# Kernel tuning notes

Hardware: AMD Instinct MI355X
Metric: run time of the kernel (lower is better)

Reference implementation:

```python
import jax, jax.numpy as jnp
import numpy as np
from jax import lax


def setup_inputs() -> dict:
    key = jax.random.key(0)
    ks = jax.random.split(key, 8)
    b, l, d_model = 2, 1024, 768
    expand, d_state, d_conv = 2, 16, 4
    d_inner = d_model * expand            # 1536
    dt_rank = -(-d_model // 16)           # ceil(768/16) = 48
    x = jax.random.normal(ks[0], (b, l, d_model), jnp.float32)
    W_in = jax.random.normal(ks[1], (d_model, 2 * d_inner), jnp.float32) * 0.02
    conv_w = jax.random.normal(ks[2], (d_inner, 1, d_conv), jnp.float32) * 0.1
    conv_b = jnp.zeros((d_inner,), jnp.float32)
    W_x = jax.random.normal(ks[3], (d_inner, dt_rank + 2 * d_state), jnp.float32) * 0.02
    W_dt = jax.random.normal(ks[4], (dt_rank, d_inner), jnp.float32) * 0.02
    b_dt = jax.random.normal(ks[5], (d_inner,), jnp.float32) * 0.02
    # A_log = log(1..d_state) broadcast over d_inner, as in the module init
    A_log = jnp.broadcast_to(jnp.log(jnp.arange(1, d_state + 1, dtype=jnp.float32)), (d_inner, d_state)).copy()
    D = jnp.ones((d_inner,), jnp.float32)
    W_out = jax.random.normal(ks[6], (d_inner, d_model), jnp.float32) * 0.02
    return {"x": x, "W_in": W_in, "conv_w": conv_w, "conv_b": conv_b, "W_x": W_x,
            "W_dt": W_dt, "b_dt": b_dt, "A_log": A_log, "D": D, "W_out": W_out}


def _silu(v):
    return v * jax.nn.sigmoid(v)


def reference(x, W_in, conv_w, conv_b, W_x, W_dt, b_dt, A_log, D, W_out):
    b, l, d_model = x.shape
    d_inner, _, d_conv = conv_w.shape
    dt_rank = W_dt.shape[0]
    n = A_log.shape[1]

    # in_proj and split into x / res paths
    x_and_res = x @ W_in                              # (b, l, 2*d_inner)
    xi, res = jnp.split(x_and_res, 2, axis=-1)

    # depthwise causal conv1d (torch pads d_conv-1 both sides then slices [:l])
    xc = jnp.transpose(xi, (0, 2, 1))                 # (b, d_inner, l)
    xc = lax.conv_general_dilated(
        xc, conv_w, window_strides=(1,), padding=[(d_conv - 1, 0)],
        dimension_numbers=("NCH", "OIH", "NCH"), feature_group_count=d_inner)
    xc = xc + conv_b[None, :, None]
    u = _silu(jnp.transpose(xc, (0, 2, 1)))           # (b, l, d_inner)

    # SSM parameters (input-dependent)
    A = -jnp.exp(A_log.astype(jnp.float32))           # (d_inner, n)
    x_dbl = u @ W_x                                   # (b, l, dt_rank + 2n)
    delta = x_dbl[..., :dt_rank]
    B = x_dbl[..., dt_rank:dt_rank + n]               # (b, l, n)
    C = x_dbl[..., dt_rank + n:]                      # (b, l, n)
    delta = jax.nn.softplus(delta @ W_dt + b_dt)      # (b, l, d_inner)

    # discretize
    deltaA = jnp.exp(delta[..., None] * A)            # (b, l, d_inner, n)
    deltaB_u = delta[..., None] * B[:, :, None, :] * u[..., None]  # (b, l, d_inner, n)

    # parallel associative scan over l: h_t = deltaA_t * h_{t-1} + deltaB_u_t
    def combine(c1, c2):
        a1, b1 = c1
        a2, b2 = c2
        return (a1 * a2, a2 * b1 + b2)

    _, hs = lax.associative_scan(combine, (deltaA, deltaB_u), axis=1)  # (b, l, d_inner, n)

    y = jnp.einsum("bldn,bln->bld", hs, C) + u * D    # (b, l, d_inner)
    y = y * _silu(res)
    out = y @ W_out                                   # (b, l, d_model)
    return out
```

## Files before the change

### kernel.cpp

```cpp
#include <hip/hip_runtime.h>
#include <math.h>

#define DI 1536
#define DM 768
#define NSTATE 16
#define DTRANK 48
#define LSEQ 1024
#define NBATCH 2
#define MROWS (NBATCH*LSEQ)
#define NXR 3072
#define NCHUNK 128
#define CLEN 8
#define SCB 128
#define DMP 16

typedef __attribute__((ext_vector_type(4))) float f32x4;
typedef __attribute__((ext_vector_type(8))) short s16x8;
typedef __attribute__((ext_vector_type(4))) unsigned int u32x4;

__device__ __forceinline__ unsigned short f2bf(float f) {
  unsigned int x = __builtin_bit_cast(unsigned int, f);
  return (unsigned short)((x + 0x7fffu + ((x >> 16) & 1u)) >> 16);
}
__device__ __forceinline__ float bf2f(unsigned short b) {
  unsigned int u = ((unsigned int)b) << 16;
  return __builtin_bit_cast(float, u);
}

__device__ __forceinline__ void gload_lds16(const void* g, void* l) {
  __builtin_amdgcn_global_load_lds(
      (const __attribute__((address_space(1))) void*)g,
      (__attribute__((address_space(3))) void*)l, 16, 0, 0);
}

__global__ __launch_bounds__(256) void prep_kernel(
    const float* __restrict__ x, const float* __restrict__ W_in,
    const float* __restrict__ W_out, const float* __restrict__ W_x,
    const float* __restrict__ A_log,
    unsigned short* __restrict__ x_bf, unsigned short* __restrict__ WinT,
    unsigned short* __restrict__ WoutT, unsigned short* __restrict__ WxT,
    float* __restrict__ negA)
{
  __shared__ float t[32][33];
  const int bid = blockIdx.x;
  const int tid = threadIdx.x;
  if (bid < 768) {
    long i = ((long)bid * 256 + tid) * 8;
    f32x4 v0 = *(const f32x4*)&x[i];
    f32x4 v1 = *(const f32x4*)&x[i + 4];
    unsigned short o[8];
    #pragma unroll
    for (int j = 0; j < 4; ++j) { o[j] = f2bf(v0[j]); o[4 + j] = f2bf(v1[j]); }
    *(u32x4*)&x_bf[i] = *(u32x4*)o;
    return;
  }
  int tx = tid & 31, ty = tid >> 5;
  if (bid >= 4368) {
    int rtile = (bid - 4368) * 32;
    #pragma unroll
    for (int i = 0; i < 4; ++i) {
      int r = ty + i * 8;
      if (tx < 16) t[r][tx] = A_log[(long)(rtile + r) * NSTATE + tx];
    }
    __syncthreads();
    #pragma unroll
    for (int i = 0; i < 2; ++i) {
      int cc = ty + i * 8;
      negA[(long)cc * DI + rtile + tx] = -__expf(t[tx][cc]);
    }
    return;
  }
  const float* in; unsigned short* out; int R, C, bx, by; bool guard = false;
  if (bid < 3072)      { int q = bid - 768;  in = W_in;  out = WinT;  R = DM; C = NXR; bx = q % 96; by = q / 96; }
  else if (bid < 4224) { int q = bid - 3072; in = W_out; out = WoutT; R = DI; C = DM;  bx = q % 24; by = q / 24; }
  else                 { int q = bid - 4224; in = W_x;   out = WxT;   R = DI; C = 80;  bx = q % 3;  by = q / 3; guard = true; }
  int ctile = bx * 32, rtile = by * 32;
  #pragma unroll
  for (int i = 0; i < 4; ++i) {
    int r = ty + i * 8;
    if (!guard || (rtile + r < R && ctile + tx < C))
      t[r][tx] = in[(long)(rtile + r) * C + ctile + tx];
  }
  __syncthreads();
  #pragma unroll
  for (int i = 0; i < 4; ++i) {
    int cc = ty + i * 8;
    if (!guard || (ctile + cc < C && rtile + tx < R))
      out[(long)(ctile + cc) * R + rtile + tx] = f2bf(t[tx][cc]);
  }
}

template<int FM, int FN, bool SPLIT>
__global__ __launch_bounds__(256) void gemm_bf16(
    const unsigned short* __restrict__ A,
    const unsigned short* __restrict__ BT,
    float* __restrict__ C,
    unsigned short* __restrict__ res_bf,
    int M, int N, int K)
{
  constexpr int BM = 32 * FM, BN = 32 * FN;
  constexpr int TM = BM / 16, TN = BN / 16;
  __shared__ unsigned short Ap[BM * 32];
  __shared__ unsigned short Bp[BN * 32];
  const int tid = threadIdx.x;
  const int lane = tid & 63, wave = tid >> 6;
  const int wr = wave >> 1, wc = wave & 1;
  const int lg = lane >> 4, lr = lane & 15;
  const int m0 = blockIdx.y * BM, n0 = blockIdx.x * BN;
  f32x4 acc[FM][FN] = {};
  for (int k0 = 0; k0 < K; k0 += 32) {
    #pragma unroll
    for (int p = 0; p < TM / 4; ++p) {
      int tile = wave + p * 4;
      gload_lds16(&A[(long)(m0 + tile * 16 + lr) * K + k0 + lg * 8], &Ap[tile * 512]);
    }
    #pragma unroll
    for (int p = 0; p < TN / 4; ++p) {
      int tile = wave + p * 4;
      gload_lds16(&BT[(long)(n0 + tile * 16 + lr) * K + k0 + lg * 8], &Bp[tile * 512]);
    }
    __syncthreads();
    s16x8 af[FM], bfr[FN];
    #pragma unroll
    for (int m = 0; m < FM; ++m)
      af[m] = *(s16x8*)&Ap[(((wr * FM + m) * 4 + lg) * 16 + lr) * 8];
    #pragma unroll
    for (int n = 0; n < FN; ++n)
      bfr[n] = *(s16x8*)&Bp[(((wc * FN + n) * 4 + lg) * 16 + lr) * 8];
    #pragma unroll
    for (int m = 0; m < FM; ++m)
      #pragma unroll
      for (int n = 0; n < FN; ++n)
        acc[m][n] = __builtin_amdgcn_mfma_f32_16x16x32_bf16(af[m], bfr[n], acc[m][n], 0, 0, 0);
    __syncthreads();
  }
  #pragma unroll
  for (int m = 0; m < FM; ++m)
    #pragma unroll
    for (int n = 0; n < FN; ++n)
      #pragma unroll
      for (int r = 0; r < 4; ++r) {
        int row = m0 + wr * 16 * FM + m * 16 + lg * 4 + r;
        int col = n0 + wc * 16 * FN + n * 16 + lr;
        if (SPLIT) {
          if (n0 < DI) C[(long)row * DI + col] = acc[m][n][r];
          else res_bf[(long)row * DI + col - DI] = f2bf(acc[m][n][r]);
        } else {
          C[(long)row * N + col] = acc[m][n][r];
        }
      }
}

__global__ __launch_bounds__(256) void conv_silu_kernel(
    const float* __restrict__ xi,
    const float* __restrict__ conv_w,
    const float* __restrict__ conv_b,
    unsigned short* __restrict__ u_bf)
{
  int idx = blockIdx.x * 256 + threadIdx.x;
  if (idx >= MROWS * DI) return;
  int c = idx % DI;
  int m = idx / DI;
  int t = m % LSEQ;
  float w0 = conv_w[c * 4 + 0], w1 = conv_w[c * 4 + 1];
  float w2 = conv_w[c * 4 + 2], w3 = conv_w[c * 4 + 3];
  float acc = conv_b[c];
  if (t >= 3) acc = fmaf(xi[(long)(m - 3) * DI + c], w0, acc);
  if (t >= 2) acc = fmaf(xi[(long)(m - 2) * DI + c], w1, acc);
  if (t >= 1) acc = fmaf(xi[(long)(m - 1) * DI + c], w2, acc);
  acc = fmaf(xi[(long)m * DI + c], w3, acc);
  float s = acc / (1.f + __expf(-acc));
  u_bf[idx] = f2bf(s);
}

__global__ __launch_bounds__(256) void xdbl_mfma(
    const unsigned short* __restrict__ u_bf,
    const unsigned short* __restrict__ WxT,
    float* __restrict__ xdbl)
{
  const int tid = threadIdx.x;
  const int lane = tid & 63, wave = tid >> 6;
  const int lg = lane >> 4, lr = lane & 15;
  const int m0 = blockIdx.x * 16;
  f32x4 acc[5] = {};
  const int kbase = wave * (DI / 4);
  #pragma unroll
  for (int kk = 0; kk < DI / 4; kk += 32) {
    int k0 = kbase + kk;
    s16x8 af = *(const s16x8*)&u_bf[(long)(m0 + lr) * DI + k0 + lg * 8];
    #pragma unroll
    for (int n = 0; n < 5; ++n) {
      s16x8 bfr = *(const s16x8*)&WxT[(long)(n * 16 + lr) * DI + k0 + lg * 8];
      acc[n] = __builtin_amdgcn_mfma_f32_16x16x32_bf16(af, bfr, acc[n], 0, 0, 0);
    }
  }
  __shared__ float red[4][16][80];
  #pragma unroll
  for (int n = 0; n < 5; ++n)
    #pragma unroll
    for (int r = 0; r < 4; ++r)
      red[wave][lg * 4 + r][n * 16 + lr] = acc[n][r];
  __syncthreads();
  for (int i = tid; i < 16 * 80; i += 256) {
    int row = i / 80, col = i % 80;
    float s = red[0][row][col] + red[1][row][col] + red[2][row][col] + red[3][row][col];
    xdbl[(long)(m0 + row) * 80 + col] = s;
  }
}

__global__ __launch_bounds__(256) void delta_kernel(
    const float* __restrict__ xdbl,
    const float* __restrict__ W_dt,
    const float* __restrict__ b_dt,
    float* __restrict__ delta)
{
  __shared__ float sx[DMP][DTRANK];
  const int tid = threadIdx.x;
  const int c = blockIdx.x * 256 + tid;
  const int m0 = blockIdx.y * DMP;
  for (int i = tid; i < DMP * DTRANK; i += 256) {
    int mm = i / DTRANK, r = i % DTRANK;
    sx[mm][r] = xdbl[(long)(m0 + mm) * 80 + r];
  }
  __syncthreads();
  float bias = b_dt[c];
  float acc[DMP];
  #pragma unroll
  for (int mm = 0; mm < DMP; ++mm) acc[mm] = bias;
  for (int r = 0; r < DTRANK; ++r) {
    float wv = W_dt[(long)r * DI + c];
    #pragma unroll
    for (int mm = 0; mm < DMP; ++mm)
      acc[mm] = fmaf(sx[mm][r], wv, acc[mm]);
  }
  #pragma unroll
  for (int mm = 0; mm < DMP; ++mm) {
    float v = acc[mm];
    float sp = (v > 20.f) ? v : log1pf(__expf(v));
    delta[(long)(m0 + mm) * DI + c] = sp;
  }
}

__global__ __launch_bounds__(SCB) void scan_ph1(
    const float* __restrict__ delta,
    const float* __restrict__ xdbl,
    const unsigned short* __restrict__ u_bf,
    const float* __restrict__ negA,
    float* __restrict__ Aprod,
    float* __restrict__ Hend)
{
  const int b = blockIdx.z, chunk = blockIdx.y;
  const int tid = threadIdx.x;
  const int d = blockIdx.x * SCB + tid;
  const long mbase = (long)b * LSEQ + chunk * CLEN;
  __shared__ float sB[CLEN][NSTATE];
  for (int i = tid; i < CLEN * NSTATE; i += SCB) {
    int t = i >> 4, j = i & 15;
    sB[t][j] = xdbl[(mbase + t) * 80 + DTRANK + j];
  }
  __syncthreads();
  float a[NSTATE];
  #pragma unroll
  for (int n = 0; n < NSTATE; ++n)
    a[n] = negA[(long)n * DI + d];
  float h[NSTATE] = {};
  float Ap[NSTATE];
  #pragma unroll
  for (int n = 0; n < NSTATE; ++n) Ap[n] = 1.f;
  #pragma unroll
  for (int t = 0; t < CLEN; ++t) {
    long m = mbase + t;
    float dt = delta[m * DI + d];
    float uu = bf2f(u_bf[m * DI + d]);
    float dtu = dt * uu;
    #pragma unroll
    for (int n = 0; n < NSTATE; ++n) {
      float dA = __expf(dt * a[n]);
      Ap[n] *= dA;
      h[n] = fmaf(dA, h[n], dtu * sB[t][n]);
    }
  }
  const long o = ((long)(b * NCHUNK + chunk) * NSTATE) * DI + d;
  #pragma unroll
  for (int n = 0; n < NSTATE; ++n) {
    Aprod[o + (long)n * DI] = Ap[n];
    Hend[o + (long)n * DI] = h[n];
  }
}

__global__ __launch_bounds__(256) void scan_ph2(
    const float* __restrict__ Aprod,
    float* __restrict__ Hend)
{
  int idx = blockIdx.x * 256 + threadIdx.x;
  int b = idx / (DI * NSTATE);
  int r = idx % (DI * NSTATE);
  long o = (long)b * NCHUNK * DI * NSTATE + r;
  const long stride = (long)DI * NSTATE;
  float h = 0.f;
  for (int c = 0; c < NCHUNK; ++c) {
    float Ap = Aprod[o + c * stride];
    float He = Hend[o + c * stride];
    Hend[o + c * stride] = h;
    h = fmaf(Ap, h, He);
  }
}

__global__ __launch_bounds__(SCB) void scan_ph3(
    const float* __restrict__ delta,
    const float* __restrict__ xdbl,
    const unsigned short* __restrict__ u_bf,
    const unsigned short* __restrict__ res_bf,
    const float* __restrict__ negA,
    const float* __restrict__ Dp,
    const float* __restrict__ Hstart,
    unsigned short* __restrict__ yg)
{
  const int b = blockIdx.z, chunk = blockIdx.y;
  const int tid = threadIdx.x;
  const int d = blockIdx.x * SCB + tid;
  const long mbase = (long)b * LSEQ + chunk * CLEN;
  __shared__ float sB[CLEN][NSTATE], sC[CLEN][NSTATE];
  for (int i = tid; i < CLEN * NSTATE; i += SCB) {
    int t = i >> 4, j = i & 15;
    long mo = (mbase + t) * 80 + DTRANK + j;
    sB[t][j] = xdbl[mo];
    sC[t][j] = xdbl[mo + NSTATE];
  }
  __syncthreads();
  float a[NSTATE];
  #pragma unroll
  for (int n = 0; n < NSTATE; ++n)
    a[n] = negA[(long)n * DI + d];
  const float Dv = Dp[d];
  const long o = ((long)(b * NCHUNK + chunk) * NSTATE) * DI + d;
  float h[NSTATE];
  #pragma unroll
  for (int n = 0; n < NSTATE; ++n)
    h[n] = Hstart[o + (long)n * DI];
  #pragma unroll
  for (int t = 0; t < CLEN; ++t) {
    long m = mbase + t;
    float dt = delta[m * DI + d];
    float uu = bf2f(u_bf[m * DI + d]);
    float rr = bf2f(res_bf[m * DI + d]);
    float dtu = dt * uu;
    float p0 = 0.f, p1 = 0.f, p2 = 0.f, p3 = 0.f;
    #pragma unroll
    for (int q = 0; q < 4; ++q) {
      float dA0 = __expf(dt * a[q*4+0]);
      float dA1 = __expf(dt * a[q*4+1]);
      float dA2 = __expf(dt * a[q*4+2]);
      float dA3 = __expf(dt * a[q*4+3]);
      h[q*4+0] = fmaf(dA0, h[q*4+0], dtu * sB[t][q*4+0]);
      h[q*4+1] = fmaf(dA1, h[q*4+1], dtu * sB[t][q*4+1]);
      h[q*4+2] = fmaf(dA2, h[q*4+2], dtu * sB[t][q*4+2]);
      h[q*4+3] = fmaf(dA3, h[q*4+3], dtu * sB[t][q*4+3]);
    }
    #pragma unroll
    for (int n = 0; n < NSTATE; n += 4) {
      p0 = fmaf(h[n+0], sC[t][n+0], p0);
      p1 = fmaf(h[n+1], sC[t][n+1], p1);
      p2 = fmaf(h[n+2], sC[t][n+2], p2);
      p3 = fmaf(h[n+3], sC[t][n+3], p3);
    }
    float yv = (p0 + p1) + (p2 + p3) + uu * Dv;
    float gate = rr / (1.f + __expf(-rr));
    yg[m * DI + d] = f2bf(yv * gate);
  }
}

extern "C" void kernel_launch(void* const* d_in, const int* in_sizes, int n_in,
                              void* d_out, int out_size, void* d_ws, size_t ws_size,
                              hipStream_t stream)
{
  const float* x      = (const float*)d_in[0];
  const float* W_in   = (const float*)d_in[1];
  const float* conv_w = (const float*)d_in[2];
  const float* conv_b = (const float*)d_in[3];
  const float* W_x    = (const float*)d_in[4];
  const float* W_dt   = (const float*)d_in[5];
  const float* b_dt   = (const float*)d_in[6];
  const float* A_log  = (const float*)d_in[7];
  const float* Dp     = (const float*)d_in[8];
  const float* W_out  = (const float*)d_in[9];
  float* out = (float*)d_out;

  char* p = (char*)d_ws;
  float* xi     = (float*)(p + 0);
  unsigned short* res_bf = (unsigned short*)(p + 12582912);
  unsigned short* u_bf   = (unsigned short*)(p + 18874368);
  float* xdbl   = (float*)(p + 25165824);
  float* delta  = (float*)(p + 25821184);
  float* Aprod  = (float*)(p + 38404096);
  float* Hend   = (float*)(p + 63569920);
  unsigned short* yg    = (unsigned short*)(p + 88735744);
  unsigned short* x_bf  = (unsigned short*)(p + 95027200);
  unsigned short* WinT  = (unsigned short*)(p + 98172928);
  unsigned short* WoutT = (unsigned short*)(p + 102891520);
  unsigned short* WxT   = (unsigned short*)(p + 105250816);
  float* negA   = (float*)(p + 105496576);

  prep_kernel<<<4416, 256, 0, stream>>>(x, W_in, W_out, W_x, A_log,
                                        x_bf, WinT, WoutT, WxT, negA);
  gemm_bf16<2, 4, true><<<dim3(NXR / 128, MROWS / 64), 256, 0, stream>>>(
      x_bf, WinT, xi, res_bf, MROWS, NXR, DM);
  conv_silu_kernel<<<(MROWS * DI + 255) / 256, 256, 0, stream>>>(
      xi, conv_w, conv_b, u_bf);
  xdbl_mfma<<<MROWS / 16, 256, 0, stream>>>(u_bf, WxT, xdbl);
  delta_kernel<<<dim3(DI / 256, MROWS / DMP), 256, 0, stream>>>(xdbl, W_dt, b_dt, delta);
  scan_ph1<<<dim3(DI / SCB, NCHUNK, NBATCH), SCB, 0, stream>>>(
      delta, xdbl, u_bf, negA, Aprod, Hend);
  scan_ph2<<<(NBATCH * DI * NSTATE) / 256, 256, 0, stream>>>(Aprod, Hend);
  scan_ph3<<<dim3(DI / SCB, NCHUNK, NBATCH), SCB, 0, stream>>>(
      delta, xdbl, u_bf, res_bf, negA, Dp, Hend, yg);
  gemm_bf16<2, 2, false><<<dim3(DM / 64, MROWS / 64), 256, 0, stream>>>(
      yg, WoutT, out, nullptr, MROWS, DM, DI);
}
```

Before: 160.7 us.

## Fuse conv+SiLU into x_dbl MFMA kernel and vectorize LDS reads

Merges the depthwise conv+SiLU kernel with the x_dbl projection. Each block computes its 16 rows of u into padded LDS and still writes u_bf to global, then feeds the MFMA from LDS instead of re-reading global memory. This removes one launch and a global round-trip for u. The delta and scan kernels now read shared B/C/x_dbl values as aligned float4 vectors. The fused kernel runs only 128 blocks for the elementwise conv work, so parallelism for that phase drops.

```diff
diff --git a/kernel.cpp b/kernel.cpp
--- a/kernel.cpp
+++ b/kernel.cpp
@@ -13,6 +13,7 @@
 #define CLEN 8
 #define SCB 128
 #define DMP 16
+#define ULDS 1544
 
 typedef __attribute__((ext_vector_type(4))) float f32x4;
 typedef __attribute__((ext_vector_type(8))) short s16x8;
@@ -151,59 +152,61 @@
       }
 }
 
-__global__ __launch_bounds__(256) void conv_silu_kernel(
+__global__ __launch_bounds__(256) void mid_kernel(
     const float* __restrict__ xi,
     const float* __restrict__ conv_w,
     const float* __restrict__ conv_b,
-    unsigned short* __restrict__ u_bf)
-{
-  int idx = blockIdx.x * 256 + threadIdx.x;
-  if (idx >= MROWS * DI) return;
-  int c = idx % DI;
-  int m = idx / DI;
-  int t = m % LSEQ;
-  float w0 = conv_w[c * 4 + 0], w1 = conv_w[c * 4 + 1];
-  float w2 = conv_w[c * 4 + 2], w3 = conv_w[c * 4 + 3];
-  float acc = conv_b[c];
-  if (t >= 3) acc = fmaf(xi[(long)(m - 3) * DI + c], w0, acc);
-  if (t >= 2) acc = fmaf(xi[(long)(m - 2) * DI + c], w1, acc);
-  if (t >= 1) acc = fmaf(xi[(long)(m - 1) * DI + c], w2, acc);
-  acc = fmaf(xi[(long)m * DI + c], w3, acc);
-  float s = acc / (1.f + __expf(-acc));
-  u_bf[idx] = f2bf(s);
-}
-
-__global__ __launch_bounds__(256) void xdbl_mfma(
-    const unsigned short* __restrict__ u_bf,
     const unsigned short* __restrict__ WxT,
+    unsigned short* __restrict__ u_bf,
     float* __restrict__ xdbl)
 {
-  const int tid = threadIdx.x;
+  __shared__ __align__(16) char smem[16 * ULDS * 2];
+  unsigned short* uL = (unsigned short*)smem;
+  float* red = (float*)smem;
+  const int tid = threadIdx.x;
+  const int m0 = blockIdx.x * 16;
+  for (int i = tid; i < 16 * DI; i += 256) {
+    int row = i / DI, col = i - row * DI;
+    int m = m0 + row;
+    int t = m % LSEQ;
+    float w0 = conv_w[col * 4 + 0], w1 = conv_w[col * 4 + 1];
+    float w2 = conv_w[col * 4 + 2], w3 = conv_w[col * 4 + 3];
+    float acc = conv_b[col];
+    if (t >= 3) acc = fmaf(xi[(long)(m - 3) * DI + col], w0, acc);
+    if (t >= 2) acc = fmaf(xi[(long)(m - 2) * DI + col], w1, acc);
+    if (t >= 1) acc = fmaf(xi[(long)(m - 1) * DI + col], w2, acc);
+    acc = fmaf(xi[(long)m * DI + col], w3, acc);
+    float s = acc / (1.f + __expf(-acc));
+    unsigned short bv = f2bf(s);
+    uL[row * ULDS + col] = bv;
+    u_bf[(long)m * DI + col] = bv;
+  }
+  __syncthreads();
   const int lane = tid & 63, wave = tid >> 6;
   const int lg = lane >> 4, lr = lane & 15;
-  const int m0 = blockIdx.x * 16;
   f32x4 acc[5] = {};
   const int kbase = wave * (DI / 4);
   #pragma unroll
   for (int kk = 0; kk < DI / 4; kk += 32) {
     int k0 = kbase + kk;
-    s16x8 af = *(const s16x8*)&u_bf[(long)(m0 + lr) * DI + k0 + lg * 8];
+    s16x8 af = *(const s16x8*)&uL[lr * ULDS + k0 + lg * 8];
     #pragma unroll
     for (int n = 0; n < 5; ++n) {
       s16x8 bfr = *(const s16x8*)&WxT[(long)(n * 16 + lr) * DI + k0 + lg * 8];
       acc[n] = __builtin_amdgcn_mfma_f32_16x16x32_bf16(af, bfr, acc[n], 0, 0, 0);
     }
   }
-  __shared__ float red[4][16][80];
+  __syncthreads();
   #pragma unroll
   for (int n = 0; n < 5; ++n)
     #pragma unroll
     for (int r = 0; r < 4; ++r)
-      red[wave][lg * 4 + r][n * 16 + lr] = acc[n][r];
+      red[(wave * 16 + lg * 4 + r) * 80 + n * 16 + lr] = acc[n][r];
   __syncthreads();
   for (int i = tid; i < 16 * 80; i += 256) {
-    int row = i / 80, col = i % 80;
-    float s = red[0][row][col] + red[1][row][col] + red[2][row][col] + red[3][row][col];
+    int row = i / 80, col = i - row * 80;
+    float s = red[(0 * 16 + row) * 80 + col] + red[(1 * 16 + row) * 80 + col]
+            + red[(2 * 16 + row) * 80 + col] + red[(3 * 16 + row) * 80 + col];
     xdbl[(long)(m0 + row) * 80 + col] = s;
   }
 }
@@ -214,7 +217,7 @@
     const float* __restrict__ b_dt,
     float* __restrict__ delta)
 {
-  __shared__ float sx[DMP][DTRANK];
+  __shared__ __align__(16) float sx[DMP][DTRANK];
   const int tid = threadIdx.x;
   const int c = blockIdx.x * 256 + tid;
   const int m0 = blockIdx.y * DMP;
@@ -227,11 +230,19 @@
   float acc[DMP];
   #pragma unroll
   for (int mm = 0; mm < DMP; ++mm) acc[mm] = bias;
-  for (int r = 0; r < DTRANK; ++r) {
-    float wv = W_dt[(long)r * DI + c];
-    #pragma unroll
-    for (int mm = 0; mm < DMP; ++mm)
-      acc[mm] = fmaf(sx[mm][r], wv, acc[mm]);
+  for (int r = 0; r < DTRANK; r += 4) {
+    float wv0 = W_dt[(long)(r + 0) * DI + c];
+    float wv1 = W_dt[(long)(r + 1) * DI + c];
+    float wv2 = W_dt[(long)(r + 2) * DI + c];
+    float wv3 = W_dt[(long)(r + 3) * DI + c];
+    #pragma unroll
+    for (int mm = 0; mm < DMP; ++mm) {
+      f32x4 s4 = *(const f32x4*)&sx[mm][r];
+      float a = fmaf(s4[0], wv0, acc[mm]);
+      a = fmaf(s4[1], wv1, a);
+      a = fmaf(s4[2], wv2, a);
+      acc[mm] = fmaf(s4[3], wv3, a);
+    }
   }
   #pragma unroll
   for (int mm = 0; mm < DMP; ++mm) {
@@ -253,7 +264,7 @@
   const int tid = threadIdx.x;
   const int d = blockIdx.x * SCB + tid;
   const long mbase = (long)b * LSEQ + chunk * CLEN;
-  __shared__ float sB[CLEN][NSTATE];
+  __shared__ __align__(16) float sB[CLEN][NSTATE];
   for (int i = tid; i < CLEN * NSTATE; i += SCB) {
     int t = i >> 4, j = i & 15;
     sB[t][j] = xdbl[(mbase + t) * 80 + DTRANK + j];
@@ -274,10 +285,15 @@
     float uu = bf2f(u_bf[m * DI + d]);
     float dtu = dt * uu;
     #pragma unroll
-    for (int n = 0; n < NSTATE; ++n) {
-      float dA = __expf(dt * a[n]);
-      Ap[n] *= dA;
-      h[n] = fmaf(dA, h[n], dtu * sB[t][n]);
+    for (int q = 0; q < 4; ++q) {
+      f32x4 b4 = *(const f32x4*)&sB[t][q * 4];
+      #pragma unroll
+      for (int j = 0; j < 4; ++j) {
+        int n = q * 4 + j;
+        float dA = __expf(dt * a[n]);
+        Ap[n] *= dA;
+        h[n] = fmaf(dA, h[n], dtu * b4[j]);
+      }
     }
   }
   const long o = ((long)(b * NCHUNK + chunk) * NSTATE) * DI + d;
@@ -320,7 +336,7 @@
   const int tid = threadIdx.x;
   const int d = blockIdx.x * SCB + tid;
   const long mbase = (long)b * LSEQ + chunk * CLEN;
-  __shared__ float sB[CLEN][NSTATE], sC[CLEN][NSTATE];
+  __shared__ __align__(16) float sB[CLEN][NSTATE], sC[CLEN][NSTATE];
   for (int i = tid; i < CLEN * NSTATE; i += SCB) {
     int t = i >> 4, j = i & 15;
     long mo = (mbase + t) * 80 + DTRANK + j;
@@ -348,21 +364,23 @@
     float p0 = 0.f, p1 = 0.f, p2 = 0.f, p3 = 0.f;
     #pragma unroll
     for (int q = 0; q < 4; ++q) {
+      f32x4 b4 = *(const f32x4*)&sB[t][q * 4];
       float dA0 = __expf(dt * a[q*4+0]);
       float dA1 = __expf(dt * a[q*4+1]);
       float dA2 = __expf(dt * a[q*4+2]);
       float dA3 = __expf(dt * a[q*4+3]);
-      h[q*4+0] = fmaf(dA0, h[q*4+0], dtu * sB[t][q*4+0]);
-      h[q*4+1] = fmaf(dA1, h[q*4+1], dtu * sB[t][q*4+1]);
-      h[q*4+2] = fmaf(dA2, h[q*4+2], dtu * sB[t][q*4+2]);
-      h[q*4+3] = fmaf(dA3, h[q*4+3], dtu * sB[t][q*4+3]);
-    }
-    #pragma unroll
-    for (int n = 0; n < NSTATE; n += 4) {
-      p0 = fmaf(h[n+0], sC[t][n+0], p0);
-      p1 = fmaf(h[n+1], sC[t][n+1], p1);
-      p2 = fmaf(h[n+2], sC[t][n+2], p2);
-      p3 = fmaf(h[n+3], sC[t][n+3], p3);
+      h[q*4+0] = fmaf(dA0, h[q*4+0], dtu * b4[0]);
+      h[q*4+1] = fmaf(dA1, h[q*4+1], dtu * b4[1]);
+      h[q*4+2] = fmaf(dA2, h[q*4+2], dtu * b4[2]);
+      h[q*4+3] = fmaf(dA3, h[q*4+3], dtu * b4[3]);
+    }
+    #pragma unroll
+    for (int q = 0; q < 4; ++q) {
+      f32x4 c4 = *(const f32x4*)&sC[t][q * 4];
+      p0 = fmaf(h[q*4+0], c4[0], p0);
+      p1 = fmaf(h[q*4+1], c4[1], p1);
+      p2 = fmaf(h[q*4+2], c4[2], p2);
+      p3 = fmaf(h[q*4+3], c4[3], p3);
     }
     float yv = (p0 + p1) + (p2 + p3) + uu * Dv;
     float gate = rr / (1.f + __expf(-rr));
@@ -405,9 +423,7 @@
                                         x_bf, WinT, WoutT, WxT, negA);
   gemm_bf16<2, 4, true><<<dim3(NXR / 128, MROWS / 64), 256, 0, stream>>>(
       x_bf, WinT, xi, res_bf, MROWS, NXR, DM);
-  conv_silu_kernel<<<(MROWS * DI + 255) / 256, 256, 0, stream>>>(
-      xi, conv_w, conv_b, u_bf);
-  xdbl_mfma<<<MROWS / 16, 256, 0, stream>>>(u_bf, WxT, xdbl);
+  mid_kernel<<<MROWS / 16, 256, 0, stream>>>(xi, conv_w, conv_b, WxT, u_bf, xdbl);
   delta_kernel<<<dim3(DI / 256, MROWS / DMP), 256, 0, stream>>>(xdbl, W_dt, b_dt, delta);
   scan_ph1<<<dim3(DI / SCB, NCHUNK, NBATCH), SCB, 0, stream>>>(
       delta, xdbl, u_bf, negA, Aprod, Hend);
```

New measurement: 324.7 us. 102% more time.
